# Performance work log

Hardware: AMD Instinct MI355X
Metric: run time of the kernel (lower is better)

Reference implementation:

```python
import jax, jax.numpy as jnp
import numpy as np

B = 4
N_SAMPLES = 32768
N_EVENTS = 32
N_HARMONICS = 16
SAMPLES_PER_FRAME = 256
N_FRAMES = N_SAMPLES // SAMPLES_PER_FRAME  # 128
SAMPLERATE = 22050
NYQ = SAMPLERATE // 2
MIN_F = 20.0 / NYQ
MAX_F = 4000.0 / NYQ
RES_BASE = 0.8
N_ROOMS = 8
LOG_SQRT_2PI = 0.5 * np.log(2.0 * np.pi).astype(np.float32)


def max_norm(x):
    return x / (jnp.max(jnp.abs(x), axis=-1, keepdims=True) + 1e-8)


def window(means, stds, n, mn, mx, eps=1e-8):
    # means/stds: [B, E, 1]; Normal pdf evaluated on linspace(0,1,n), max-normalized
    mu = mn + means * (mx - mn)
    sigma = eps + stds
    rng = jnp.linspace(0.0, 1.0, n, dtype=jnp.float32)[None, None, :]
    logp = -0.5 * ((rng - mu) / sigma) ** 2 - jnp.log(sigma) - LOG_SQRT_2PI
    return max_norm(jnp.exp(logp))


def interp_linear(x, out_size):
    # F.interpolate(mode='linear', align_corners=False) along last axis
    in_size = x.shape[-1]
    coords = (jnp.arange(out_size, dtype=jnp.float32) + 0.5) * (in_size / out_size) - 0.5
    coords = jnp.clip(coords, 0.0, in_size - 1.0)
    lo = jnp.floor(coords).astype(jnp.int32)
    hi = jnp.minimum(lo + 1, in_size - 1)
    w = (coords - lo.astype(jnp.float32))
    return x[..., lo] * (1.0 - w) + x[..., hi] * w


def fft_convolve(a, b):
    # zero-padded linear convolution via FFT, truncated to original length
    n = a.shape[-1]
    pa = jnp.pad(a, [(0, 0)] * (a.ndim - 1) + [(0, n)])
    pb = jnp.pad(b, [(0, 0)] * (b.ndim - 1) + [(0, n)])
    out = jnp.fft.irfft(jnp.fft.rfft(pa) * jnp.fft.rfft(pb), n=2 * n)
    return out[..., :n]


def setup_inputs():
    key = jax.random.key(0)
    k1, k2, k3, k4, k5 = jax.random.split(key, 5)
    return {
        'event_params': jax.random.uniform(k1, (B, N_EVENTS, N_HARMONICS + 6), dtype=jnp.float32),
        'mx_raw': jax.random.normal(k2, (B,), dtype=jnp.float32),
        'room_logits': jax.random.normal(k3, (B, N_ROOMS), dtype=jnp.float32),
        'noise': jax.random.uniform(k4, (1, 1, N_SAMPLES), dtype=jnp.float32, minval=-1.0, maxval=1.0),
        'impulse_responses': jax.random.normal(k5, (N_ROOMS, N_SAMPLES), dtype=jnp.float32) * 0.01,
    }


def reference(event_params, mx_raw, room_logits, noise, impulse_responses):
    b = event_params.shape[0]
    ep = event_params  # [B, E, 22], already in [0,1] (post-activation)
    freq_means = ep[:, :, 0:1] ** 2
    freq_stds = ep[:, :, 1:2] * 0.1
    time_means = ep[:, :, 2:3]
    time_stds = ep[:, :, 3:4] * 0.1
    f0 = ep[:, :, 4:5] ** 2
    amps = ep[:, :, 5:6] ** 2
    res = ep[:, :, 6:] * (1.0 - RES_BASE) + RES_BASE  # [B, E, H]
    mx = jax.nn.sigmoid(mx_raw).reshape(b, 1, 1)
    rooms = jax.nn.softmax(room_logits, axis=-1)

    # --- BandLimitedNoise ---
    nfft = N_SAMPLES // 2 + 1
    win = window(freq_means, freq_stds, nfft, MIN_F, MAX_F)  # [B, E, nfft]
    noise_spec = jnp.fft.rfft(noise, norm='ortho')            # [1, 1, nfft]
    bl_noise = jnp.fft.irfft(noise_spec * win, n=N_SAMPLES, norm='ortho')  # [B, E, N]

    # --- impulse (time) windows ---
    events = window(time_means, time_stds, N_SAMPLES, 0.0, 1.0)  # [B, E, N]

    # --- Resonance ---
    factors = jnp.arange(1, N_HARMONICS + 1, dtype=jnp.float32)
    f0s = MIN_F + (MAX_F - MIN_F) * f0                 # [B, E, 1]
    freqs = f0s * factors                               # [B, E, H]
    freqs = jnp.where(freqs >= 1.0, 0.0, freqs)
    freqs_fr = jnp.broadcast_to(freqs[..., None], freqs.shape + (N_FRAMES,))
    freqs_s = interp_linear(freqs_fr, N_SAMPLES)        # [B, E, H, N]
    res_fr = jnp.cumprod(jnp.broadcast_to(res[..., None], res.shape + (N_FRAMES,)), axis=-1)
    res_s = interp_linear(res_fr, N_SAMPLES)            # [B, E, H, N]
    resonances = jnp.sum(res_s * jnp.sin(jnp.cumsum(freqs_s * (2.0 * np.pi), axis=-1)), axis=2)  # [B, E, N]

    # --- locate events + resonance convolution (noise_coeff = 1) ---
    located = bl_noise * events * amps
    located = fft_convolve(located, resonances) + located
    located = jnp.sum(located, axis=1, keepdims=True)   # [B, 1, N]

    # --- reverb: rooms-weighted impulse response, dry/wet mix ---
    dry = located
    imp = jnp.einsum('br,rn->bn', rooms, impulse_responses)[:, None, :]
    wet = fft_convolve(located, imp)
    return dry * (1.0 - mx) + wet * mx
```

## Files before the change

### kernel.cpp

```cpp
#include <hip/hip_runtime.h>
#include <math.h>

#define NSAMP 32768
#define NPAD  65536
#define NCH   128
#define TWO_PI 6.2831853071795864f
#define MINF ((float)(20.0/11025.0))
#define DRF  ((float)(4000.0/11025.0 - 20.0/11025.0))

__device__ __forceinline__ float2 cxmul(float2 a, float2 b){
    return make_float2(a.x*b.x - a.y*b.y, a.x*b.y + a.y*b.x);
}

template<int DIR>
__device__ __forceinline__ void fft4v(float2* v, int i0, int i1, int i2, int i3){
    float2 a=v[i0], b=v[i1], c=v[i2], d=v[i3];
    float2 t0 = make_float2(a.x+c.x, a.y+c.y);
    float2 t1 = make_float2(a.x-c.x, a.y-c.y);
    float2 t2 = make_float2(b.x+d.x, b.y+d.y);
    float2 t3 = make_float2(b.x-d.x, b.y-d.y);
    v[i0] = make_float2(t0.x+t2.x, t0.y+t2.y);
    v[i2] = make_float2(t0.x-t2.x, t0.y-t2.y);
    if (DIR < 0) {
        v[i1] = make_float2(t1.x + t3.y, t1.y - t3.x);
        v[i3] = make_float2(t1.x - t3.y, t1.y + t3.x);
    } else {
        v[i1] = make_float2(t1.x - t3.y, t1.y + t3.x);
        v[i3] = make_float2(t1.x + t3.y, t1.y - t3.x);
    }
}

template<int DIR>
__device__ __forceinline__ void twm(float2& v, float c, float s){
    float sy = (DIR<0) ? -s : s;
    v = cxmul(v, make_float2(c, sy));
}

template<int DIR>
__device__ __forceinline__ void fft16r(float2* v){
    const float C1=0.92387953251128674f, S1=0.38268343236508978f, H=0.70710678118654752f;
    fft4v<DIR>(v,0,4,8,12);
    fft4v<DIR>(v,1,5,9,13);
    fft4v<DIR>(v,2,6,10,14);
    fft4v<DIR>(v,3,7,11,15);
    twm<DIR>(v[5],  C1, S1);
    twm<DIR>(v[6],  H,  H);
    twm<DIR>(v[7],  S1, C1);
    twm<DIR>(v[9],  H,  H);
    twm<DIR>(v[10], 0.0f, 1.0f);
    twm<DIR>(v[11], -H, H);
    twm<DIR>(v[13], S1, C1);
    twm<DIR>(v[14], -H, H);
    twm<DIR>(v[15], -C1, -S1);
    fft4v<DIR>(v,0,1,2,3);
    fft4v<DIR>(v,4,5,6,7);
    fft4v<DIR>(v,8,9,10,11);
    fft4v<DIR>(v,12,13,14,15);
}

template<int DIR>
__device__ __forceinline__ void fft8r(float2* v){
    const float H=0.70710678118654752f;
    #pragma unroll
    for (int n1=0;n1<4;n1++){
        float2 t=v[n1], u=v[n1+4];
        v[n1]   = make_float2(t.x+u.x, t.y+u.y);
        v[n1+4] = make_float2(t.x-u.x, t.y-u.y);
    }
    twm<DIR>(v[5], H, H);
    twm<DIR>(v[6], 0.0f, 1.0f);
    twm<DIR>(v[7], -H, H);
    fft4v<DIR>(v,0,1,2,3);
    fft4v<DIR>(v,4,5,6,7);
}

__device__ __forceinline__ int slot16(int r){ return ((r&3)<<2)|(r>>2); }
__device__ __forceinline__ int slot8(int r){ return ((r&1)<<2)|(r>>1); }
__device__ __forceinline__ int lpad(int l){ return l + (l>>4); }

template<int R>
__device__ __forceinline__ void twiddle(float2* v, float ang1){
    float s,c; __sincosf(ang1,&s,&c);
    float2 w[R];
    w[1] = make_float2(c,s);
    #pragma unroll
    for (int r=2;r<R;r++) w[r] = cxmul(w[r>>1], w[r-(r>>1)]);
    #pragma unroll
    for (int r=1;r<R;r++) v[r] = cxmul(v[r], w[r]);
}

template<int DIR>
__device__ __forceinline__ void n1_tail(float2 (&v)[16], float2* lds, int t, int p,
                                        float2* __restrict__ out)
{
    fft16r<DIR>(v);
    #pragma unroll
    for (int r=0;r<16;r++) lds[lpad(256*(t>>4) + 16*(t&15) + r)] = v[slot16(r)];
    __syncthreads();
    #pragma unroll
    for (int q=0;q<16;q++) v[q] = lds[lpad(256*q + t)];
    int jm = t & 15;
    if (jm) twiddle<16>(v, (DIR<0?-TWO_PI:TWO_PI)*(float)jm*(1.0f/256.0f));
    fft16r<DIR>(v);
    int j2 = 256*p + t;
    float2* yo = out + (j2>>4)*256 + (j2&15);
    #pragma unroll
    for (int r=0;r<16;r++) yo[16*r] = v[slot16(r)];
}

__global__ __launch_bounds__(256) void mfk_n1_noise_setup(const float* __restrict__ noise,
        float2* __restrict__ dst, const float* __restrict__ EP,
        const float* __restrict__ MXR, const float* __restrict__ RL,
        float* __restrict__ chP, unsigned* __restrict__ chQ, float* __restrict__ cum,
        float* __restrict__ mxA, float* __restrict__ rmA)
{
    __shared__ float2 lds[4352];
    int t = threadIdx.x, px = blockIdx.x;
    if (px >= 8){
        int q = (px-8)*256 + t;
        int c = q >> 4, h = q & 15;
        const float* P = EP + c*22;
        const float LSQ = (float)0.9189385332046727;
        float f0m = __fmul_rn(P[4],P[4]);
        float f0s = __fadd_rn(MINF, __fmul_rn(f0m, DRF));
        float fr  = __fmul_rn(f0s, (float)(h+1));
        if (fr >= 1.0f) fr = 0.0f;
        chQ[q] = (unsigned)(unsigned long long)((double)fr*4294967296.0 + 0.5);
        float rs = __fadd_rn(__fmul_rn(P[6+h],0.2f),0.8f);
        float cp = rs;
        float* crow = cum + (size_t)q*128;
        for (int jj=0;jj<128;jj++){ crow[jj] = cp; cp = __fmul_rn(cp, rs); }
        if (h == 0){
            float fm  = __fmul_rn(P[0],P[0]);
            float fmu = __fadd_rn(MINF, __fmul_rn(fm, DRF));
            float fsg = 1e-8f + P[1]*0.1f;
            float fsi = 1.0f/fsg;
            int i0 = (int)floorf(fmu*16384.0f + 0.5f);
            i0 = min(max(i0,0),16384);
            float rg = (float)i0 * (1.0f/16384.0f);
            float tt = (rg - fmu)*fsi;
            float Lc = logf(fsg) + LSQ;
            float sc = expf(-Lc) / (expf(-0.5f*tt*tt - Lc) + 1e-8f);
            float tmu = P[2];
            float tsg = 1e-8f + P[3]*0.1f;
            float tsi = 1.0f/tsg;
            int i1 = (int)floorf(tmu*32767.0f + 0.5f);
            i1 = min(max(i1,0),32767);
            float rg1 = (float)((double)i1 * (1.0/32767.0));
            float tt1 = (rg1 - tmu)*tsi;
            float Lc1 = logf(tsg) + LSQ;
            float sc1 = expf(-Lc1) / (expf(-0.5f*tt1*tt1 - Lc1) + 1e-8f);
            float amp = P[5]*P[5];
            float* o = chP + c*8;
            o[0]=fmu; o[1]=fsi; o[2]=sc; o[3]=tmu; o[4]=tsi; o[5]=sc1; o[6]=amp; o[7]=0.f;
        }
        if (q < 4){
            int b = q;
            mxA[b] = 1.0f/(1.0f + expf(-MXR[b]));
            const float* rl = RL + b*8;
            float mx = rl[0];
            for (int r=1;r<8;r++) mx = fmaxf(mx, rl[r]);
            float sum=0.f;
            float e2[8];
            for (int r=0;r<8;r++){ e2[r]=expf(rl[r]-mx); sum+=e2[r]; }
            for (int r=0;r<8;r++) rmA[b*8+r] = e2[r]/sum;
        }
        return;
    }
    int p = px;
    int j = 128*(t>>4) + 16*p + (t&15);
    float2 v[16];
    #pragma unroll
    for (int r=0;r<16;r++) v[r] = make_float2(noise[j + 2048*r], 0.0f);
    n1_tail<-1>(v, lds, t, p, dst);
}

__global__ __launch_bounds__(256) void mfk_n1_specwin(const float2* __restrict__ nspec,
        const float* __restrict__ chP, float2* __restrict__ dst, int g0)
{
    __shared__ float2 lds[4352];
    int t = threadIdx.x, p = blockIdx.x, pr = blockIdx.y;
    int c0 = g0 + 2*pr;
    const float* A = chP + c0*8;
    const float* B = chP + (c0+1)*8;
    float a0=A[0], a1=A[1], a2=A[2], b0=B[0], b1=B[1], b2=B[2];
    int j = 128*(t>>4) + 16*p + (t&15);
    float2 v[16];
    #pragma unroll
    for (int r=0;r<16;r++){
        int k = j + 2048*r;
        int kw = (k <= 16384) ? k : (32768 - k);
        float rg = (float)kw * (1.0f/16384.0f);
        float t0 = (rg - a0)*a1;
        float w0 = expf(-0.5f*t0*t0)*a2;
        float t1 = (rg - b0)*b1;
        float w1 = expf(-0.5f*t1*t1)*b2;
        float2 N = nspec[k];
        v[r] = make_float2(N.x*w0 - N.y*w1, N.y*w0 + N.x*w1);
    }
    n1_tail<1>(v, lds, t, p, dst + (size_t)pr*NSAMP);
}

template<int DIR>
__device__ __forceinline__ void n2_stageC(const float2* __restrict__ x, float2* lds, int t, int p)
{
    float2 v[16];
    int j2 = 256*(t>>5) + 32*p + (t&31);
    #pragma unroll
    for (int r=0;r<16;r++) v[r] = x[j2 + 2048*r];
    int jm = 32*p + (t&31);
    if (jm) twiddle<16>(v, (DIR<0?-TWO_PI:TWO_PI)*(float)jm*(1.0f/4096.0f));
    fft16r<DIR>(v);
    #pragma unroll
    for (int r=0;r<16;r++) lds[lpad(256*r + t)] = v[slot16(r)];
    __syncthreads();
}

template<int DIR>
__device__ __forceinline__ int n2_stageD(float2* lds, int t, int p, int u, float2 (&w8)[8])
{
    int q = t + 256*u;
    int j3 = ((q>>5)<<8) + 32*p + (q&31);
    #pragma unroll
    for (int r3=0;r3<8;r3++) w8[r3] = lds[lpad(256*(q>>5) + 32*r3 + (q&31))];
    if (j3) twiddle<8>(w8, (DIR<0?-TWO_PI:TWO_PI)*(float)j3*(1.0f/32768.0f));
    fft8r<DIR>(w8);
    return j3;
}

__global__ __launch_bounds__(256) void mfk_n2_noise(const float2* __restrict__ src,
                                                    float2* __restrict__ dst)
{
    __shared__ float2 lds[4352];
    int t = threadIdx.x, p = blockIdx.x;
    n2_stageC<-1>(src, lds, t, p);
    #pragma unroll
    for (int u=0;u<2;u++){
        float2 w8[8];
        int j3 = n2_stageD<-1>(lds, t, p, u, w8);
        #pragma unroll
        for (int r=0;r<8;r++) dst[j3 + 4096*r] = w8[slot8(r)];
    }
}

__global__ __launch_bounds__(256) void mfk_n2_unpack(const float2* __restrict__ src,
        const float* __restrict__ chP, float* __restrict__ locraw, int g0)
{
    __shared__ float2 lds[4352];
    int t = threadIdx.x, p = blockIdx.x, pr = blockIdx.y;
    n2_stageC<1>(src + (size_t)pr*NSAMP, lds, t, p);
    int lc0 = 2*pr;
    const float* C0 = chP + (g0+lc0)*8;
    const float* C1 = chP + (g0+lc0+1)*8;
    float c03=C0[3], c04=C0[4], c05=C0[5], c06=C0[6];
    float c13=C1[3], c14=C1[4], c15=C1[5], c16=C1[6];
    #pragma unroll
    for (int u=0;u<2;u++){
        float2 w8[8];
        int j3 = n2_stageD<1>(lds, t, p, u, w8);
        #pragma unroll
        for (int r=0;r<8;r++){
            int n = j3 + 4096*r;
            float2 val = w8[slot8(r)];
            float rg = (float)((double)n * (1.0/32767.0));
            float tt0 = (rg - c03)*c04;
            float ew0 = expf(-0.5f*tt0*tt0)*c05;
            float tt1 = (rg - c13)*c14;
            float ew1 = expf(-0.5f*tt1*tt1)*c15;
            locraw[(size_t)lc0*NSAMP + n]     = val.x*(1.0f/32768.0f)*ew0*c06;
            locraw[(size_t)(lc0+1)*NSAMP + n] = val.y*(1.0f/32768.0f)*ew1*c16;
        }
    }
}

__global__ __launch_bounds__(256) void mfk_packZres_f01(const float* __restrict__ locraw,
        const unsigned* __restrict__ chQ, const float* __restrict__ cum,
        float2* __restrict__ dst, int g0)
{
    __shared__ float2 lds[4352];
    __shared__ unsigned qS[16];
    float* cumS = (float*)lds;
    int t = threadIdx.x, p = blockIdx.x, lc = blockIdx.y;
    int cg = g0 + lc;
    const float* crow = cum + (size_t)cg*2048;
    #pragma unroll
    for (int i=0;i<8;i++) cumS[t + 256*i] = crow[t + 256*i];
    if (t < 16) qS[t] = chQ[cg*16 + t];
    __syncthreads();
    int j = 256*(t>>4) + 16*p + (t&15);
    const float* la = locraw + (size_t)lc*NSAMP;
    float2 v[16];
    #pragma unroll
    for (int r=0;r<8;r++){
        int n = j + 4096*r;
        float co = ((float)n + 0.5f)*0.00390625f - 0.5f;
        co = fminf(fmaxf(co,0.0f),127.0f);
        int lo = (int)co;
        float wf = co - (float)lo;
        int hi = min(lo+1,127);
        unsigned T1 = (unsigned)(n+1);
        float acc = (n==0) ? 1.0f : 0.0f;
        #pragma unroll
        for (int hh=0; hh<16; hh++){
            float e0 = cumS[hh*128+lo], e1 = cumS[hh*128+hi];
            float env = e0 + (e1-e0)*wf;
            unsigned bits = qS[hh]*T1;
            float m = (float)bits * 2.3283064365386963e-10f;
            float sv; asm("v_sin_f32 %0, %1" : "=v"(sv) : "v"(m));
            acc = fmaf(env, sv, acc);
        }
        v[r] = make_float2(la[n], acc);
    }
    #pragma unroll
    for (int r=8;r<16;r++) v[r] = make_float2(0.f,0.f);
    __syncthreads();
    n1_tail<-1>(v, lds, t, p, dst + (size_t)lc*NPAD);
}

__global__ __launch_bounds__(256) void mfk_prod_f01(const float2* __restrict__ Z,
        float2* __restrict__ dst)
{
    __shared__ float2 lds[4352];
    int t = threadIdx.x;
    int px = blockIdx.x;
    int p = (px < 8) ? px : 23 - px;
    int pr = blockIdx.y;
    const float2* z0 = Z + (size_t)(2*pr)*NPAD;
    const float2* z1 = z0 + NPAD;
    int j = 256*(t>>4) + 16*p + (t&15);
    float2 v[16];
    #pragma unroll
    for (int r=0;r<16;r++){
        int k = j + 4096*r;
        int km = (NPAD - k) & (NPAD-1);
        float2 a = z0[k], am = z0[km];
        float2 A0 = make_float2(0.5f*(a.x+am.x), 0.5f*(a.y-am.y));
        float2 R0 = make_float2(0.5f*(a.y+am.y), -0.5f*(a.x-am.x));
        float2 P0 = cxmul(A0,R0);
        float2 b = z1[k], bm = z1[km];
        float2 A1 = make_float2(0.5f*(b.x+bm.x), 0.5f*(b.y-bm.y));
        float2 R1 = make_float2(0.5f*(b.y+bm.y), -0.5f*(b.x-bm.x));
        float2 P1 = cxmul(A1,R1);
        const float s = 1.0f/65536.0f;
        v[r] = make_float2((P0.x - P1.y)*s, (P0.y + P1.x)*s);
    }
    n1_tail<1>(v, lds, t, p, dst + (size_t)pr*NPAD);
}

__global__ __launch_bounds__(256) void mfk_dryacc_f01(const float2* __restrict__ U,
        const float* __restrict__ rmA, const float* __restrict__ IR,
        float* __restrict__ located, float2* __restrict__ dst)
{
    __shared__ float2 lds[4352];
    int t = threadIdx.x, p = blockIdx.x, b = blockIdx.y;
    int j = 256*(t>>4) + 16*p + (t&15);
    float rm[8];
    #pragma unroll
    for (int r=0;r<8;r++) rm[r] = rmA[b*8+r];
    float2 v[16];
    #pragma unroll
    for (int r=0;r<8;r++){
        int n = j + 4096*r;
        float sum = 0.f;
        #pragma unroll
        for (int e=0;e<16;e++){
            float2 u = U[(size_t)(16*b+e)*NPAD + n];
            sum += u.x + u.y;
        }
        located[(size_t)b*NSAMP + n] = sum;
        float iv = 0.f;
        #pragma unroll
        for (int q=0;q<8;q++) iv += rm[q]*IR[(size_t)q*NSAMP + n];
        v[r] = make_float2(sum, iv);
    }
    #pragma unroll
    for (int r=8;r<16;r++) v[r] = make_float2(0.f,0.f);
    n1_tail<-1>(v, lds, t, p, dst + (size_t)b*NPAD);
}

__global__ __launch_bounds__(256) void mfk_dry_f01(const float* __restrict__ located,
        const float* __restrict__ rmA, const float* __restrict__ IR, float2* __restrict__ dst)
{
    __shared__ float2 lds[4352];
    int t = threadIdx.x, p = blockIdx.x, b = blockIdx.y;
    int j = 256*(t>>4) + 16*p + (t&15);
    float rm[8];
    #pragma unroll
    for (int r=0;r<8;r++) rm[r] = rmA[b*8+r];
    float2 v[16];
    #pragma unroll
    for (int r=0;r<8;r++){
        int n = j + 4096*r;
        float iv = 0.f;
        #pragma unroll
        for (int q=0;q<8;q++) iv += rm[q]*IR[(size_t)q*NSAMP + n];
        v[r] = make_float2(located[(size_t)b*NSAMP + n], iv);
    }
    #pragma unroll
    for (int r=8;r<16;r++) v[r] = make_float2(0.f,0.f);
    n1_tail<-1>(v, lds, t, p, dst + (size_t)b*NPAD);
}

template<int DIR, int NSTORE>
__global__ __launch_bounds__(256) void mfk_f23(const float2* __restrict__ src,
                                               float2* __restrict__ dst)
{
    __shared__ float2 lds[4352];
    int t = threadIdx.x, p = blockIdx.x;
    size_t boff = (size_t)blockIdx.y * NPAD;
    int a = t>>4, w = t&15;
    int j = 256*a + 16*p + w;
    const float2* x = src + boff;
    float2 v[16];
    #pragma unroll
    for (int r=0;r<16;r++) v[r] = x[j + 4096*r];
    int jm = 16*p + w;
    if (jm) twiddle<16>(v, (DIR<0?-TWO_PI:TWO_PI)*(float)jm*(1.0f/4096.0f));
    fft16r<DIR>(v);
    #pragma unroll
    for (int r=0;r<16;r++) lds[lpad(256*a + 16*r + w)] = v[slot16(r)];
    __syncthreads();
    #pragma unroll
    for (int q=0;q<16;q++) v[q] = lds[lpad(256*q + t)];
    if (j) twiddle<16>(v, (DIR<0?-TWO_PI:TWO_PI)*(float)j*(1.0f/65536.0f));
    fft16r<DIR>(v);
    float2* yo = dst + boff + j;
    #pragma unroll
    for (int r=0;r<NSTORE;r++) yo[4096*r] = v[slot16(r)];
}

__global__ __launch_bounds__(256) void mfk_f23_final(const float2* __restrict__ src,
        const float* __restrict__ located, const float* __restrict__ mxA,
        float* __restrict__ out)
{
    __shared__ float2 lds[4352];
    int t = threadIdx.x, p = blockIdx.x;
    size_t boff = (size_t)blockIdx.y * NPAD;
    int a = t>>4, w = t&15;
    int j = 256*a + 16*p + w;
    const float2* x = src + boff;
    float2 v[16];
    #pragma unroll
    for (int r=0;r<16;r++) v[r] = x[j + 4096*r];
    int jm = 16*p + w;
    if (jm) twiddle<16>(v, TWO_PI*(float)jm*(1.0f/4096.0f));
    fft16r<1>(v);
    #pragma unroll
    for (int r=0;r<16;r++) lds[lpad(256*a + 16*r + w)] = v[slot16(r)];
    __syncthreads();
    #pragma unroll
    for (int q=0;q<16;q++) v[q] = lds[lpad(256*q + t)];
    if (j) twiddle<16>(v, TWO_PI*(float)j*(1.0f/65536.0f));
    fft16r<1>(v);
    int b0 = 2*blockIdx.y, b1 = b0+1;
    float mx0 = mxA[b0], mx1 = mxA[b1];
    #pragma unroll
    for (int r=0;r<8;r++){
        int ts = j + 4096*r;
        float2 val = v[slot16(r)];
        out[(size_t)b0*NSAMP+ts] = located[(size_t)b0*NSAMP+ts]*(1.f-mx0) + val.x*mx0;
        out[(size_t)b1*NSAMP+ts] = located[(size_t)b1*NSAMP+ts]*(1.f-mx1) + val.y*mx1;
    }
}

__global__ __launch_bounds__(256) void mfk_accum(const float2* __restrict__ U,
        float* __restrict__ located, int g0, int eStart, int eCount, int bBase, int addTo)
{
    int t = blockIdx.x*256 + threadIdx.x;
    int b = bBase + blockIdx.y;
    float sum = 0.f;
    for (int ei=0; ei<eCount; ei++){
        int lc = b*32 + eStart + ei - g0;
        float2 u = U[(size_t)(lc>>1)*NPAD + t];
        sum += (lc & 1) ? u.y : u.x;
    }
    size_t idx = (size_t)b*NSAMP + t;
    float base0 = addTo ? located[idx] : 0.0f;
    located[idx] = base0 + sum;
}

extern "C" void kernel_launch(void* const* d_in, const int* in_sizes, int n_in,
                              void* d_out, int out_size, void* d_ws, size_t ws_size,
                              hipStream_t stream)
{
    (void)in_sizes; (void)n_in; (void)out_size;
    const float* EP   = (const float*)d_in[0];
    const float* MXR  = (const float*)d_in[1];
    const float* RL   = (const float*)d_in[2];
    const float* NOISE= (const float*)d_in[3];
    const float* IR   = (const float*)d_in[4];
    float* out = (float*)d_out;
    char* w = (char*)d_ws;

    auto need = [](long long g)->long long {
        return 2LL*g*NPAD*8 + 1LL*g*NSAMP*4 + (long long)NSAMP*8
             + 2048LL*128*4 + (128LL*8 + 2048 + 4 + 32 + 4LL*NSAMP)*4 + 16384;
    };
    int G = 128;
    while (G > 4 && need(G) > (long long)ws_size) G >>= 1;

    size_t off = 0;
    auto alloc = [&](size_t bytes)->char* {
        char* p = w + off; off += (bytes + 255) & ~(size_t)255; return p;
    };
    float2*   arA    = (float2*)alloc((size_t)G*NPAD*8);
    float2*   arB    = (float2*)alloc((size_t)G*NPAD*8);
    float*    locraw = (float*) alloc((size_t)G*NSAMP*4);
    float2*   nspec  = (float2*)alloc((size_t)NSAMP*8);
    float*    cum    = (float*) alloc(2048LL*128*4);
    float*    chP    = (float*) alloc(128*8*4);
    unsigned* chQ    = (unsigned*)alloc(2048*4);
    float*    mxA    = (float*) alloc(4*4);
    float*    rmA    = (float*) alloc(32*4);
    float*    located= (float*) alloc(4*NSAMP*4);

    mfk_n1_noise_setup<<<dim3(16),256,0,stream>>>(NOISE, arB, EP, MXR, RL,
                                                  chP, chQ, cum, mxA, rmA);
    mfk_n2_noise<<<dim3(8),256,0,stream>>>(arB, nspec);

    for (int g0 = 0; g0 < NCH; g0 += G){
        int P = G/2;
        mfk_n1_specwin<<<dim3(8,P),256,0,stream>>>(nspec, chP, arA, g0);
        mfk_n2_unpack<<<dim3(8,P),256,0,stream>>>(arA, chP, locraw, g0);
        mfk_packZres_f01<<<dim3(16,G),256,0,stream>>>(locraw, chQ, cum, arA, g0);
        mfk_f23<-1,16><<<dim3(16,G),256,0,stream>>>(arA, arB);
        mfk_prod_f01<<<dim3(16,P),256,0,stream>>>(arB, arA);
        mfk_f23<1,8><<<dim3(16,P),256,0,stream>>>(arA, arB);
        if (G < NCH){
            int bBase, bCnt, eStart, eCount;
            if (G >= 32){ bBase = g0/32; bCnt = G/32; eStart = 0; eCount = 32; }
            else        { bBase = g0/32; bCnt = 1; eStart = g0 % 32; eCount = G; }
            int addTo = (eStart != 0);
            mfk_accum<<<dim3(128,bCnt),256,0,stream>>>(arB, located, g0, eStart, eCount, bBase, addTo);
        }
    }

    if (G == NCH){
        mfk_dryacc_f01<<<dim3(16,4),256,0,stream>>>(arB, rmA, IR, located, arA);
    } else {
        mfk_dry_f01<<<dim3(16,4),256,0,stream>>>(located, rmA, IR, arA);
    }
    mfk_f23<-1,16><<<dim3(16,4),256,0,stream>>>(arA, arB);
    mfk_prod_f01<<<dim3(16,2),256,0,stream>>>(arB, arA);
    mfk_f23_final<<<dim3(16,2),256,0,stream>>>(arA, located, mxA, out);
}
```

Baseline: 185.5 us.

## Halve LDS footprint by transposing in two half passes and raise occupancy

The 16x256 shared-memory transpose in the FFT kernels now runs in two halves over a buffer half the size, with extra barriers between the halves. The n2 kernels likewise stage their data in two halves. Several kernels also get a minimum-blocks-per-SM launch bound of 6. The aim is more resident workgroups per CU to hide global-memory latency, at the cost of extra synchronisation and possible register pressure or spills from the launch-bound hint.

```diff
diff --git a/kernel.cpp b/kernel.cpp
--- a/kernel.cpp
+++ b/kernel.cpp
@@ -78,6 +78,8 @@
 __device__ __forceinline__ int slot8(int r){ return ((r&1)<<2)|(r>>1); }
 __device__ __forceinline__ int lpad(int l){ return l + (l>>4); }
 
+#define LDSN 2176
+
 template<int R>
 __device__ __forceinline__ void twiddle(float2* v, float ang1){
     float s,c; __sincosf(ang1,&s,&c);
@@ -89,23 +91,41 @@
     for (int r=1;r<R;r++) v[r] = cxmul(v[r], w[r]);
 }
 
+template<int COLMODE>
+__device__ __forceinline__ void xpose16(float2 (&v)[16], float2 (&w)[16], float2* lds, int t)
+{
+    int row = t>>4, lane = t&15;
+    #pragma unroll
+    for (int half=0; half<2; half++){
+        if (half) __syncthreads();
+        if ((row>>3) == half){
+            int rb = 256*(row&7);
+            #pragma unroll
+            for (int r=0;r<16;r++){
+                int col = COLMODE ? (16*r + lane) : (16*lane + r);
+                lds[lpad(rb + col)] = v[slot16(r)];
+            }
+        }
+        __syncthreads();
+        #pragma unroll
+        for (int q=0;q<8;q++) w[8*half + q] = lds[lpad(256*q + t)];
+    }
+}
+
 template<int DIR>
 __device__ __forceinline__ void n1_tail(float2 (&v)[16], float2* lds, int t, int p,
                                         float2* __restrict__ out)
 {
     fft16r<DIR>(v);
-    #pragma unroll
-    for (int r=0;r<16;r++) lds[lpad(256*(t>>4) + 16*(t&15) + r)] = v[slot16(r)];
-    __syncthreads();
-    #pragma unroll
-    for (int q=0;q<16;q++) v[q] = lds[lpad(256*q + t)];
+    float2 w[16];
+    xpose16<0>(v, w, lds, t);
     int jm = t & 15;
-    if (jm) twiddle<16>(v, (DIR<0?-TWO_PI:TWO_PI)*(float)jm*(1.0f/256.0f));
-    fft16r<DIR>(v);
+    if (jm) twiddle<16>(w, (DIR<0?-TWO_PI:TWO_PI)*(float)jm*(1.0f/256.0f));
+    fft16r<DIR>(w);
     int j2 = 256*p + t;
     float2* yo = out + (j2>>4)*256 + (j2&15);
     #pragma unroll
-    for (int r=0;r<16;r++) yo[16*r] = v[slot16(r)];
+    for (int r=0;r<16;r++) yo[16*r] = w[slot16(r)];
 }
 
 __global__ __launch_bounds__(256) void mfk_n1_noise_setup(const float* __restrict__ noise,
@@ -114,7 +134,7 @@
         float* __restrict__ chP, unsigned* __restrict__ chQ, float* __restrict__ cum,
         float* __restrict__ mxA, float* __restrict__ rmA)
 {
-    __shared__ float2 lds[4352];
+    __shared__ float2 lds[LDSN];
     int t = threadIdx.x, px = blockIdx.x;
     if (px >= 8){
         int q = (px-8)*256 + t;
@@ -175,10 +195,10 @@
     n1_tail<-1>(v, lds, t, p, dst);
 }
 
-__global__ __launch_bounds__(256) void mfk_n1_specwin(const float2* __restrict__ nspec,
+__global__ __launch_bounds__(256,6) void mfk_n1_specwin(const float2* __restrict__ nspec,
         const float* __restrict__ chP, float2* __restrict__ dst, int g0)
 {
-    __shared__ float2 lds[4352];
+    __shared__ float2 lds[LDSN];
     int t = threadIdx.x, p = blockIdx.x, pr = blockIdx.y;
     int c0 = g0 + 2*pr;
     const float* A = chP + c0*8;
@@ -202,18 +222,14 @@
 }
 
 template<int DIR>
-__device__ __forceinline__ void n2_stageC(const float2* __restrict__ x, float2* lds, int t, int p)
-{
-    float2 v[16];
+__device__ __forceinline__ void n2_head(const float2* __restrict__ x, float2 (&v)[16], int t, int p)
+{
     int j2 = 256*(t>>5) + 32*p + (t&31);
     #pragma unroll
     for (int r=0;r<16;r++) v[r] = x[j2 + 2048*r];
     int jm = 32*p + (t&31);
     if (jm) twiddle<16>(v, (DIR<0?-TWO_PI:TWO_PI)*(float)jm*(1.0f/4096.0f));
     fft16r<DIR>(v);
-    #pragma unroll
-    for (int r=0;r<16;r++) lds[lpad(256*r + t)] = v[slot16(r)];
-    __syncthreads();
 }
 
 template<int DIR>
@@ -222,20 +238,25 @@
     int q = t + 256*u;
     int j3 = ((q>>5)<<8) + 32*p + (q&31);
     #pragma unroll
-    for (int r3=0;r3<8;r3++) w8[r3] = lds[lpad(256*(q>>5) + 32*r3 + (q&31))];
+    for (int r3=0;r3<8;r3++) w8[r3] = lds[lpad(256*((q>>5)&7) + 32*r3 + (q&31))];
     if (j3) twiddle<8>(w8, (DIR<0?-TWO_PI:TWO_PI)*(float)j3*(1.0f/32768.0f));
     fft8r<DIR>(w8);
     return j3;
 }
 
-__global__ __launch_bounds__(256) void mfk_n2_noise(const float2* __restrict__ src,
-                                                    float2* __restrict__ dst)
-{
-    __shared__ float2 lds[4352];
+__global__ __launch_bounds__(256,6) void mfk_n2_noise(const float2* __restrict__ src,
+                                                      float2* __restrict__ dst)
+{
+    __shared__ float2 lds[LDSN];
     int t = threadIdx.x, p = blockIdx.x;
-    n2_stageC<-1>(src, lds, t, p);
+    float2 v[16];
+    n2_head<-1>(src, v, t, p);
     #pragma unroll
     for (int u=0;u<2;u++){
+        if (u) __syncthreads();
+        #pragma unroll
+        for (int r=0;r<8;r++) lds[lpad(256*r + t)] = v[slot16(8*u + r)];
+        __syncthreads();
         float2 w8[8];
         int j3 = n2_stageD<-1>(lds, t, p, u, w8);
         #pragma unroll
@@ -243,12 +264,13 @@
     }
 }
 
-__global__ __launch_bounds__(256) void mfk_n2_unpack(const float2* __restrict__ src,
+__global__ __launch_bounds__(256,6) void mfk_n2_unpack(const float2* __restrict__ src,
         const float* __restrict__ chP, float* __restrict__ locraw, int g0)
 {
-    __shared__ float2 lds[4352];
+    __shared__ float2 lds[LDSN];
     int t = threadIdx.x, p = blockIdx.x, pr = blockIdx.y;
-    n2_stageC<1>(src + (size_t)pr*NSAMP, lds, t, p);
+    float2 v[16];
+    n2_head<1>(src + (size_t)pr*NSAMP, v, t, p);
     int lc0 = 2*pr;
     const float* C0 = chP + (g0+lc0)*8;
     const float* C1 = chP + (g0+lc0+1)*8;
@@ -256,6 +278,10 @@
     float c13=C1[3], c14=C1[4], c15=C1[5], c16=C1[6];
     #pragma unroll
     for (int u=0;u<2;u++){
+        if (u) __syncthreads();
+        #pragma unroll
+        for (int r=0;r<8;r++) lds[lpad(256*r + t)] = v[slot16(8*u + r)];
+        __syncthreads();
         float2 w8[8];
         int j3 = n2_stageD<1>(lds, t, p, u, w8);
         #pragma unroll
@@ -277,7 +303,7 @@
         const unsigned* __restrict__ chQ, const float* __restrict__ cum,
         float2* __restrict__ dst, int g0)
 {
-    __shared__ float2 lds[4352];
+    __shared__ float2 lds[LDSN];
     __shared__ unsigned qS[16];
     float* cumS = (float*)lds;
     int t = threadIdx.x, p = blockIdx.x, lc = blockIdx.y;
@@ -317,10 +343,10 @@
     n1_tail<-1>(v, lds, t, p, dst + (size_t)lc*NPAD);
 }
 
-__global__ __launch_bounds__(256) void mfk_prod_f01(const float2* __restrict__ Z,
+__global__ __launch_bounds__(256,6) void mfk_prod_f01(const float2* __restrict__ Z,
         float2* __restrict__ dst)
 {
-    __shared__ float2 lds[4352];
+    __shared__ float2 lds[LDSN];
     int t = threadIdx.x;
     int px = blockIdx.x;
     int p = (px < 8) ? px : 23 - px;
@@ -351,7 +377,7 @@
         const float* __restrict__ rmA, const float* __restrict__ IR,
         float* __restrict__ located, float2* __restrict__ dst)
 {
-    __shared__ float2 lds[4352];
+    __shared__ float2 lds[LDSN];
     int t = threadIdx.x, p = blockIdx.x, b = blockIdx.y;
     int j = 256*(t>>4) + 16*p + (t&15);
     float rm[8];
@@ -381,7 +407,7 @@
 __global__ __launch_bounds__(256) void mfk_dry_f01(const float* __restrict__ located,
         const float* __restrict__ rmA, const float* __restrict__ IR, float2* __restrict__ dst)
 {
-    __shared__ float2 lds[4352];
+    __shared__ float2 lds[LDSN];
     int t = threadIdx.x, p = blockIdx.x, b = blockIdx.y;
     int j = 256*(t>>4) + 16*p + (t&15);
     float rm[8];
@@ -402,62 +428,54 @@
 }
 
 template<int DIR, int NSTORE>
-__global__ __launch_bounds__(256) void mfk_f23(const float2* __restrict__ src,
-                                               float2* __restrict__ dst)
-{
-    __shared__ float2 lds[4352];
+__global__ __launch_bounds__(256,6) void mfk_f23(const float2* __restrict__ src,
+                                                 float2* __restrict__ dst)
+{
+    __shared__ float2 lds[LDSN];
     int t = threadIdx.x, p = blockIdx.x;
     size_t boff = (size_t)blockIdx.y * NPAD;
-    int a = t>>4, w = t&15;
-    int j = 256*a + 16*p + w;
+    int j = 256*(t>>4) + 16*p + (t&15);
     const float2* x = src + boff;
     float2 v[16];
     #pragma unroll
     for (int r=0;r<16;r++) v[r] = x[j + 4096*r];
-    int jm = 16*p + w;
+    int jm = 16*p + (t&15);
     if (jm) twiddle<16>(v, (DIR<0?-TWO_PI:TWO_PI)*(float)jm*(1.0f/4096.0f));
     fft16r<DIR>(v);
-    #pragma unroll
-    for (int r=0;r<16;r++) lds[lpad(256*a + 16*r + w)] = v[slot16(r)];
-    __syncthreads();
-    #pragma unroll
-    for (int q=0;q<16;q++) v[q] = lds[lpad(256*q + t)];
-    if (j) twiddle<16>(v, (DIR<0?-TWO_PI:TWO_PI)*(float)j*(1.0f/65536.0f));
-    fft16r<DIR>(v);
+    float2 w[16];
+    xpose16<1>(v, w, lds, t);
+    if (j) twiddle<16>(w, (DIR<0?-TWO_PI:TWO_PI)*(float)j*(1.0f/65536.0f));
+    fft16r<DIR>(w);
     float2* yo = dst + boff + j;
     #pragma unroll
-    for (int r=0;r<NSTORE;r++) yo[4096*r] = v[slot16(r)];
-}
-
-__global__ __launch_bounds__(256) void mfk_f23_final(const float2* __restrict__ src,
+    for (int r=0;r<NSTORE;r++) yo[4096*r] = w[slot16(r)];
+}
+
+__global__ __launch_bounds__(256,6) void mfk_f23_final(const float2* __restrict__ src,
         const float* __restrict__ located, const float* __restrict__ mxA,
         float* __restrict__ out)
 {
-    __shared__ float2 lds[4352];
+    __shared__ float2 lds[LDSN];
     int t = threadIdx.x, p = blockIdx.x;
     size_t boff = (size_t)blockIdx.y * NPAD;
-    int a = t>>4, w = t&15;
-    int j = 256*a + 16*p + w;
+    int j = 256*(t>>4) + 16*p + (t&15);
     const float2* x = src + boff;
     float2 v[16];
     #pragma unroll
     for (int r=0;r<16;r++) v[r] = x[j + 4096*r];
-    int jm = 16*p + w;
+    int jm = 16*p + (t&15);
     if (jm) twiddle<16>(v, TWO_PI*(float)jm*(1.0f/4096.0f));
     fft16r<1>(v);
-    #pragma unroll
-    for (int r=0;r<16;r++) lds[lpad(256*a + 16*r + w)] = v[slot16(r)];
-    __syncthreads();
-    #pragma unroll
-    for (int q=0;q<16;q++) v[q] = lds[lpad(256*q + t)];
-    if (j) twiddle<16>(v, TWO_PI*(float)j*(1.0f/65536.0f));
-    fft16r<1>(v);
+    float2 w[16];
+    xpose16<1>(v, w, lds, t);
+    if (j) twiddle<16>(w, TWO_PI*(float)j*(1.0f/65536.0f));
+    fft16r<1>(w);
     int b0 = 2*blockIdx.y, b1 = b0+1;
     float mx0 = mxA[b0], mx1 = mxA[b1];
     #pragma unroll
     for (int r=0;r<8;r++){
         int ts = j + 4096*r;
-        float2 val = v[slot16(r)];
+        float2 val = w[slot16(r)];
         out[(size_t)b0*NSAMP+ts] = located[(size_t)b0*NSAMP+ts]*(1.f-mx0) + val.x*mx0;
         out[(size_t)b1*NSAMP+ts] = located[(size_t)b1*NSAMP+ts]*(1.f-mx1) + val.y*mx1;
     }
```

Result: slower. 196.4 us (+5.9%).

## Sum event spectra in frequency domain before a single inverse FFT per batch

Applied to the files above, without the earlier changes.

Instead of running an inverse 64K FFT for every channel pair and then summing events in time domain, the per-channel spectral products are accumulated across events in frequency space (mfk_prodacc), so only one inverse FFT per batch pair is needed. The dry signal is kept as packed complex pairs and reused by the reverb stage and the final mix, which removes the separate accumulation kernels. LDS padding is also replaced with an XOR swizzle, shrinking shared memory per block. This trades a large amount of inverse-FFT work for a strided spectral reduction that reads both k and N-k for every channel.

```diff
diff --git a/kernel.cpp b/kernel.cpp
--- a/kernel.cpp
+++ b/kernel.cpp
@@ -76,7 +76,7 @@
 
 __device__ __forceinline__ int slot16(int r){ return ((r&3)<<2)|(r>>2); }
 __device__ __forceinline__ int slot8(int r){ return ((r&1)<<2)|(r>>1); }
-__device__ __forceinline__ int lpad(int l){ return l + (l>>4); }
+__device__ __forceinline__ int lxs(int l){ return l ^ ((l>>4)&15); }
 
 template<int R>
 __device__ __forceinline__ void twiddle(float2* v, float ang1){
@@ -95,10 +95,10 @@
 {
     fft16r<DIR>(v);
     #pragma unroll
-    for (int r=0;r<16;r++) lds[lpad(256*(t>>4) + 16*(t&15) + r)] = v[slot16(r)];
+    for (int r=0;r<16;r++) lds[lxs(256*(t>>4) + 16*(t&15) + r)] = v[slot16(r)];
     __syncthreads();
     #pragma unroll
-    for (int q=0;q<16;q++) v[q] = lds[lpad(256*q + t)];
+    for (int q=0;q<16;q++) v[q] = lds[lxs(256*q + t)];
     int jm = t & 15;
     if (jm) twiddle<16>(v, (DIR<0?-TWO_PI:TWO_PI)*(float)jm*(1.0f/256.0f));
     fft16r<DIR>(v);
@@ -114,7 +114,7 @@
         float* __restrict__ chP, unsigned* __restrict__ chQ, float* __restrict__ cum,
         float* __restrict__ mxA, float* __restrict__ rmA)
 {
-    __shared__ float2 lds[4352];
+    __shared__ float2 lds[4096];
     int t = threadIdx.x, px = blockIdx.x;
     if (px >= 8){
         int q = (px-8)*256 + t;
@@ -178,7 +178,7 @@
 __global__ __launch_bounds__(256) void mfk_n1_specwin(const float2* __restrict__ nspec,
         const float* __restrict__ chP, float2* __restrict__ dst, int g0)
 {
-    __shared__ float2 lds[4352];
+    __shared__ float2 lds[4096];
     int t = threadIdx.x, p = blockIdx.x, pr = blockIdx.y;
     int c0 = g0 + 2*pr;
     const float* A = chP + c0*8;
@@ -212,7 +212,7 @@
     if (jm) twiddle<16>(v, (DIR<0?-TWO_PI:TWO_PI)*(float)jm*(1.0f/4096.0f));
     fft16r<DIR>(v);
     #pragma unroll
-    for (int r=0;r<16;r++) lds[lpad(256*r + t)] = v[slot16(r)];
+    for (int r=0;r<16;r++) lds[lxs(256*r + t)] = v[slot16(r)];
     __syncthreads();
 }
 
@@ -222,7 +222,7 @@
     int q = t + 256*u;
     int j3 = ((q>>5)<<8) + 32*p + (q&31);
     #pragma unroll
-    for (int r3=0;r3<8;r3++) w8[r3] = lds[lpad(256*(q>>5) + 32*r3 + (q&31))];
+    for (int r3=0;r3<8;r3++) w8[r3] = lds[lxs(256*(q>>5) + 32*r3 + (q&31))];
     if (j3) twiddle<8>(w8, (DIR<0?-TWO_PI:TWO_PI)*(float)j3*(1.0f/32768.0f));
     fft8r<DIR>(w8);
     return j3;
@@ -231,7 +231,7 @@
 __global__ __launch_bounds__(256) void mfk_n2_noise(const float2* __restrict__ src,
                                                     float2* __restrict__ dst)
 {
-    __shared__ float2 lds[4352];
+    __shared__ float2 lds[4096];
     int t = threadIdx.x, p = blockIdx.x;
     n2_stageC<-1>(src, lds, t, p);
     #pragma unroll
@@ -246,7 +246,7 @@
 __global__ __launch_bounds__(256) void mfk_n2_unpack(const float2* __restrict__ src,
         const float* __restrict__ chP, float* __restrict__ locraw, int g0)
 {
-    __shared__ float2 lds[4352];
+    __shared__ float2 lds[4096];
     int t = threadIdx.x, p = blockIdx.x, pr = blockIdx.y;
     n2_stageC<1>(src + (size_t)pr*NSAMP, lds, t, p);
     int lc0 = 2*pr;
@@ -277,9 +277,9 @@
         const unsigned* __restrict__ chQ, const float* __restrict__ cum,
         float2* __restrict__ dst, int g0)
 {
-    __shared__ float2 lds[4352];
-    __shared__ unsigned qS[16];
+    __shared__ float2 lds[4096];
     float* cumS = (float*)lds;
+    unsigned* qS = (unsigned*)(cumS + 2048);
     int t = threadIdx.x, p = blockIdx.x, lc = blockIdx.y;
     int cg = g0 + lc;
     const float* crow = cum + (size_t)cg*2048;
@@ -317,10 +317,111 @@
     n1_tail<-1>(v, lds, t, p, dst + (size_t)lc*NPAD);
 }
 
+template<int DIR, int NSTORE>
+__global__ __launch_bounds__(256) void mfk_f23(const float2* __restrict__ src,
+                                               float2* __restrict__ dst)
+{
+    __shared__ float2 lds[4096];
+    int t = threadIdx.x, p = blockIdx.x;
+    size_t boff = (size_t)blockIdx.y * NPAD;
+    int a = t>>4, w = t&15;
+    int j = 256*a + 16*p + w;
+    const float2* x = src + boff;
+    float2 v[16];
+    #pragma unroll
+    for (int r=0;r<16;r++) v[r] = x[j + 4096*r];
+    int jm = 16*p + w;
+    if (jm) twiddle<16>(v, (DIR<0?-TWO_PI:TWO_PI)*(float)jm*(1.0f/4096.0f));
+    fft16r<DIR>(v);
+    #pragma unroll
+    for (int r=0;r<16;r++) lds[lxs(256*a + 16*r + w)] = v[slot16(r)];
+    __syncthreads();
+    #pragma unroll
+    for (int q=0;q<16;q++) v[q] = lds[lxs(256*q + t)];
+    if (j) twiddle<16>(v, (DIR<0?-TWO_PI:TWO_PI)*(float)j*(1.0f/65536.0f));
+    fft16r<DIR>(v);
+    float2* yo = dst + boff + j;
+    #pragma unroll
+    for (int r=0;r<NSTORE;r++) yo[4096*r] = v[slot16(r)];
+}
+
+__global__ __launch_bounds__(256) void mfk_prodacc(const float2* __restrict__ Z,
+        float2* __restrict__ T, int g0, int G, int addTo)
+{
+    int x = blockIdx.x;
+    int beta = blockIdx.y;
+    int z = blockIdx.z;
+    int g = ((x>>4)<<3) | (x&7);
+    int kb = (x&8) ? (255 - g) : g;
+    int k = kb*256 + threadIdx.x;
+    int km = (NPAD - k) & (NPAD-1);
+    int cstart = max(64*beta + 32*z, g0);
+    int cend   = min(64*beta + 32*z + 32, g0+G);
+    float2 S0 = make_float2(0.f,0.f), S1 = make_float2(0.f,0.f);
+    #pragma unroll 4
+    for (int c=cstart; c<cend; ++c){
+        const float2* zp = Z + (size_t)(c-g0)*NPAD;
+        float2 a = zp[k], am = zp[km];
+        float2 A0 = make_float2(0.5f*(a.x+am.x), 0.5f*(a.y-am.y));
+        float2 R0 = make_float2(0.5f*(a.y+am.y), -0.5f*(a.x-am.x));
+        float2 P = cxmul(A0,R0);
+        if ((c>>5)&1){ S1.x += P.x; S1.y += P.y; }
+        else         { S0.x += P.x; S0.y += P.y; }
+    }
+    const float s = 1.0f/65536.0f;
+    float2 q = make_float2((S0.x - S1.y)*s, (S0.y + S1.x)*s);
+    size_t idx = ((size_t)z*2 + beta)*NPAD + k;
+    if (addTo){ float2 o = T[idx]; q.x += o.x; q.y += o.y; }
+    T[idx] = q;
+}
+
+__global__ __launch_bounds__(256) void mfk_plain_f01(const float2* __restrict__ T,
+        float2* __restrict__ dst)
+{
+    __shared__ float2 lds[4096];
+    int t = threadIdx.x, p = blockIdx.x, b = blockIdx.y;
+    const float2* x0 = T + (size_t)b*NPAD;
+    const float2* x1 = T + (size_t)(2+b)*NPAD;
+    int j = 256*(t>>4) + 16*p + (t&15);
+    float2 v[16];
+    #pragma unroll
+    for (int r=0;r<16;r++){
+        float2 u0 = x0[j + 4096*r], u1 = x1[j + 4096*r];
+        v[r] = make_float2(u0.x+u1.x, u0.y+u1.y);
+    }
+    n1_tail<1>(v, lds, t, p, dst + (size_t)b*NPAD);
+}
+
+__global__ __launch_bounds__(256) void mfk_dry_f01(const float2* __restrict__ U2,
+        const float* __restrict__ rmA, const float* __restrict__ IR, float2* __restrict__ dst)
+{
+    __shared__ float2 lds[4096];
+    int t = threadIdx.x, p = blockIdx.x, b = blockIdx.y;
+    int j = 256*(t>>4) + 16*p + (t&15);
+    float rm[8];
+    #pragma unroll
+    for (int r=0;r<8;r++) rm[r] = rmA[b*8+r];
+    const float2* Ub = U2 + (size_t)(b>>1)*NPAD;
+    float2 v[16];
+    #pragma unroll
+    for (int r=0;r<8;r++){
+        int n = j + 4096*r;
+        float2 lcv = Ub[n];
+        float locv = (b&1) ? lcv.y : lcv.x;
+        float iv = 0.f;
+        #pragma unroll
+        for (int q=0;q<8;q++) iv += rm[q]*IR[(size_t)q*NSAMP + n];
+        v[r] = make_float2(locv, iv);
+    }
+    #pragma unroll
+    for (int r=8;r<16;r++) v[r] = make_float2(0.f,0.f);
+    n1_tail<-1>(v, lds, t, p, dst + (size_t)b*NPAD);
+}
+
 __global__ __launch_bounds__(256) void mfk_prod_f01(const float2* __restrict__ Z,
         float2* __restrict__ dst)
 {
-    __shared__ float2 lds[4352];
+    __shared__ float2 lds[4096];
     int t = threadIdx.x;
     int px = blockIdx.x;
     int p = (px < 8) ? px : 23 - px;
@@ -347,95 +448,14 @@
     n1_tail<1>(v, lds, t, p, dst + (size_t)pr*NPAD);
 }
 
-__global__ __launch_bounds__(256) void mfk_dryacc_f01(const float2* __restrict__ U,
-        const float* __restrict__ rmA, const float* __restrict__ IR,
-        float* __restrict__ located, float2* __restrict__ dst)
-{
-    __shared__ float2 lds[4352];
-    int t = threadIdx.x, p = blockIdx.x, b = blockIdx.y;
-    int j = 256*(t>>4) + 16*p + (t&15);
-    float rm[8];
-    #pragma unroll
-    for (int r=0;r<8;r++) rm[r] = rmA[b*8+r];
-    float2 v[16];
-    #pragma unroll
-    for (int r=0;r<8;r++){
-        int n = j + 4096*r;
-        float sum = 0.f;
-        #pragma unroll
-        for (int e=0;e<16;e++){
-            float2 u = U[(size_t)(16*b+e)*NPAD + n];
-            sum += u.x + u.y;
-        }
-        located[(size_t)b*NSAMP + n] = sum;
-        float iv = 0.f;
-        #pragma unroll
-        for (int q=0;q<8;q++) iv += rm[q]*IR[(size_t)q*NSAMP + n];
-        v[r] = make_float2(sum, iv);
-    }
-    #pragma unroll
-    for (int r=8;r<16;r++) v[r] = make_float2(0.f,0.f);
-    n1_tail<-1>(v, lds, t, p, dst + (size_t)b*NPAD);
-}
-
-__global__ __launch_bounds__(256) void mfk_dry_f01(const float* __restrict__ located,
-        const float* __restrict__ rmA, const float* __restrict__ IR, float2* __restrict__ dst)
-{
-    __shared__ float2 lds[4352];
-    int t = threadIdx.x, p = blockIdx.x, b = blockIdx.y;
-    int j = 256*(t>>4) + 16*p + (t&15);
-    float rm[8];
-    #pragma unroll
-    for (int r=0;r<8;r++) rm[r] = rmA[b*8+r];
-    float2 v[16];
-    #pragma unroll
-    for (int r=0;r<8;r++){
-        int n = j + 4096*r;
-        float iv = 0.f;
-        #pragma unroll
-        for (int q=0;q<8;q++) iv += rm[q]*IR[(size_t)q*NSAMP + n];
-        v[r] = make_float2(located[(size_t)b*NSAMP + n], iv);
-    }
-    #pragma unroll
-    for (int r=8;r<16;r++) v[r] = make_float2(0.f,0.f);
-    n1_tail<-1>(v, lds, t, p, dst + (size_t)b*NPAD);
-}
-
-template<int DIR, int NSTORE>
-__global__ __launch_bounds__(256) void mfk_f23(const float2* __restrict__ src,
-                                               float2* __restrict__ dst)
-{
-    __shared__ float2 lds[4352];
+__global__ __launch_bounds__(256) void mfk_f23_final(const float2* __restrict__ src,
+        const float2* __restrict__ U2, const float* __restrict__ mxA,
+        float* __restrict__ out)
+{
+    __shared__ float2 lds[4096];
     int t = threadIdx.x, p = blockIdx.x;
-    size_t boff = (size_t)blockIdx.y * NPAD;
-    int a = t>>4, w = t&15;
-    int j = 256*a + 16*p + w;
-    const float2* x = src + boff;
-    float2 v[16];
-    #pragma unroll
-    for (int r=0;r<16;r++) v[r] = x[j + 4096*r];
-    int jm = 16*p + w;
-    if (jm) twiddle<16>(v, (DIR<0?-TWO_PI:TWO_PI)*(float)jm*(1.0f/4096.0f));
-    fft16r<DIR>(v);
-    #pragma unroll
-    for (int r=0;r<16;r++) lds[lpad(256*a + 16*r + w)] = v[slot16(r)];
-    __syncthreads();
-    #pragma unroll
-    for (int q=0;q<16;q++) v[q] = lds[lpad(256*q + t)];
-    if (j) twiddle<16>(v, (DIR<0?-TWO_PI:TWO_PI)*(float)j*(1.0f/65536.0f));
-    fft16r<DIR>(v);
-    float2* yo = dst + boff + j;
-    #pragma unroll
-    for (int r=0;r<NSTORE;r++) yo[4096*r] = v[slot16(r)];
-}
-
-__global__ __launch_bounds__(256) void mfk_f23_final(const float2* __restrict__ src,
-        const float* __restrict__ located, const float* __restrict__ mxA,
-        float* __restrict__ out)
-{
-    __shared__ float2 lds[4352];
-    int t = threadIdx.x, p = blockIdx.x;
-    size_t boff = (size_t)blockIdx.y * NPAD;
+    int pr = blockIdx.y;
+    size_t boff = (size_t)pr * NPAD;
     int a = t>>4, w = t&15;
     int j = 256*a + 16*p + w;
     const float2* x = src + boff;
@@ -446,37 +466,23 @@
     if (jm) twiddle<16>(v, TWO_PI*(float)jm*(1.0f/4096.0f));
     fft16r<1>(v);
     #pragma unroll
-    for (int r=0;r<16;r++) lds[lpad(256*a + 16*r + w)] = v[slot16(r)];
+    for (int r=0;r<16;r++) lds[lxs(256*a + 16*r + w)] = v[slot16(r)];
     __syncthreads();
     #pragma unroll
-    for (int q=0;q<16;q++) v[q] = lds[lpad(256*q + t)];
+    for (int q=0;q<16;q++) v[q] = lds[lxs(256*q + t)];
     if (j) twiddle<16>(v, TWO_PI*(float)j*(1.0f/65536.0f));
     fft16r<1>(v);
-    int b0 = 2*blockIdx.y, b1 = b0+1;
+    int b0 = 2*pr, b1 = b0+1;
     float mx0 = mxA[b0], mx1 = mxA[b1];
+    const float2* Ub = U2 + (size_t)pr*NPAD;
     #pragma unroll
     for (int r=0;r<8;r++){
         int ts = j + 4096*r;
         float2 val = v[slot16(r)];
-        out[(size_t)b0*NSAMP+ts] = located[(size_t)b0*NSAMP+ts]*(1.f-mx0) + val.x*mx0;
-        out[(size_t)b1*NSAMP+ts] = located[(size_t)b1*NSAMP+ts]*(1.f-mx1) + val.y*mx1;
-    }
-}
-
-__global__ __launch_bounds__(256) void mfk_accum(const float2* __restrict__ U,
-        float* __restrict__ located, int g0, int eStart, int eCount, int bBase, int addTo)
-{
-    int t = blockIdx.x*256 + threadIdx.x;
-    int b = bBase + blockIdx.y;
-    float sum = 0.f;
-    for (int ei=0; ei<eCount; ei++){
-        int lc = b*32 + eStart + ei - g0;
-        float2 u = U[(size_t)(lc>>1)*NPAD + t];
-        sum += (lc & 1) ? u.y : u.x;
-    }
-    size_t idx = (size_t)b*NSAMP + t;
-    float base0 = addTo ? located[idx] : 0.0f;
-    located[idx] = base0 + sum;
+        float2 dry = Ub[ts];
+        out[(size_t)b0*NSAMP+ts] = dry.x*(1.f-mx0) + val.x*mx0;
+        out[(size_t)b1*NSAMP+ts] = dry.y*(1.f-mx1) + val.y*mx1;
+    }
 }
 
 extern "C" void kernel_launch(void* const* d_in, const int* in_sizes, int n_in,
@@ -494,7 +500,8 @@
 
     auto need = [](long long g)->long long {
         return 2LL*g*NPAD*8 + 1LL*g*NSAMP*4 + (long long)NSAMP*8
-             + 2048LL*128*4 + (128LL*8 + 2048 + 4 + 32 + 4LL*NSAMP)*4 + 16384;
+             + 2048LL*128*4 + (128LL*8 + 2048 + 4 + 32)*4
+             + 4LL*NPAD*8  + 2LL*NPAD*8  + 16384;
     };
     int G = 128;
     while (G > 4 && need(G) > (long long)ws_size) G >>= 1;
@@ -506,13 +513,14 @@
     float2*   arA    = (float2*)alloc((size_t)G*NPAD*8);
     float2*   arB    = (float2*)alloc((size_t)G*NPAD*8);
     float*    locraw = (float*) alloc((size_t)G*NSAMP*4);
+    float2*   T      = (float2*)alloc(4LL*NPAD*8);
+    float2*   U2     = (float2*)alloc(2LL*NPAD*8);
     float2*   nspec  = (float2*)alloc((size_t)NSAMP*8);
     float*    cum    = (float*) alloc(2048LL*128*4);
     float*    chP    = (float*) alloc(128*8*4);
     unsigned* chQ    = (unsigned*)alloc(2048*4);
     float*    mxA    = (float*) alloc(4*4);
     float*    rmA    = (float*) alloc(32*4);
-    float*    located= (float*) alloc(4*NSAMP*4);
 
     mfk_n1_noise_setup<<<dim3(16),256,0,stream>>>(NOISE, arB, EP, MXR, RL,
                                                   chP, chQ, cum, mxA, rmA);
@@ -524,23 +532,14 @@
         mfk_n2_unpack<<<dim3(8,P),256,0,stream>>>(arA, chP, locraw, g0);
         mfk_packZres_f01<<<dim3(16,G),256,0,stream>>>(locraw, chQ, cum, arA, g0);
         mfk_f23<-1,16><<<dim3(16,G),256,0,stream>>>(arA, arB);
-        mfk_prod_f01<<<dim3(16,P),256,0,stream>>>(arB, arA);
-        mfk_f23<1,8><<<dim3(16,P),256,0,stream>>>(arA, arB);
-        if (G < NCH){
-            int bBase, bCnt, eStart, eCount;
-            if (G >= 32){ bBase = g0/32; bCnt = G/32; eStart = 0; eCount = 32; }
-            else        { bBase = g0/32; bCnt = 1; eStart = g0 % 32; eCount = G; }
-            int addTo = (eStart != 0);
-            mfk_accum<<<dim3(128,bCnt),256,0,stream>>>(arB, located, g0, eStart, eCount, bBase, addTo);
-        }
-    }
-
-    if (G == NCH){
-        mfk_dryacc_f01<<<dim3(16,4),256,0,stream>>>(arB, rmA, IR, located, arA);
-    } else {
-        mfk_dry_f01<<<dim3(16,4),256,0,stream>>>(located, rmA, IR, arA);
-    }
+        mfk_prodacc<<<dim3(256,2,2),256,0,stream>>>(arB, T, g0, G, (g0>0)?1:0);
+    }
+
+    mfk_plain_f01<<<dim3(16,2),256,0,stream>>>(T, arB);
+    mfk_f23<1,8><<<dim3(16,2),256,0,stream>>>(arB, U2);
+
+    mfk_dry_f01<<<dim3(16,4),256,0,stream>>>(U2, rmA, IR, arA);
     mfk_f23<-1,16><<<dim3(16,4),256,0,stream>>>(arA, arB);
     mfk_prod_f01<<<dim3(16,2),256,0,stream>>>(arB, arA);
-    mfk_f23_final<<<dim3(16,2),256,0,stream>>>(arA, located, mxA, out);
-}
+    mfk_f23_final<<<dim3(16,2),256,0,stream>>>(arA, U2, mxA, out);
+}
```

Result: no change. 182.1 us (-1.8%).
